# Performance work log

Measured on AMD Instinct MI355X. Metric: run time of the kernel, lower is better.

The kernel has to match this reference:

```python
import jax, jax.numpy as jnp
import numpy as np

HIDDEN = 2048
HEADS = 16
HEAD_DIM = HIDDEN // HEADS
BATCH = 2
SEQ = 2048
ROPE_BASE = 10000.0


def _rope_cos_sin(seq_len, head_dim, dtype):
    inv_freq = 1.0 / (ROPE_BASE ** (jnp.arange(0, head_dim, 2, dtype=jnp.float32) / head_dim))
    t = jnp.arange(seq_len, dtype=jnp.float32)
    freqs = jnp.outer(t, inv_freq)                 # [S, D/2]
    emb = jnp.concatenate([freqs, freqs], axis=-1)  # [S, D]
    return jnp.cos(emb).astype(dtype), jnp.sin(emb).astype(dtype)


def _rotate_half(x):
    x1, x2 = jnp.split(x, 2, axis=-1)
    return jnp.concatenate([-x2, x1], axis=-1)


def setup_inputs() -> dict:
    key = jax.random.key(0)
    ks = jax.random.split(key, 5)
    scale = 1.0 / np.sqrt(HIDDEN)
    return {
        "x": jax.random.normal(ks[0], (BATCH, SEQ, HIDDEN), dtype=jnp.float32),
        "Wq": jax.random.normal(ks[1], (HIDDEN, HIDDEN), dtype=jnp.float32) * scale,
        "Wk": jax.random.normal(ks[2], (HIDDEN, HIDDEN), dtype=jnp.float32) * scale,
        "Wv": jax.random.normal(ks[3], (HIDDEN, HIDDEN), dtype=jnp.float32) * scale,
        "Wo": jax.random.normal(ks[4], (HIDDEN, HIDDEN), dtype=jnp.float32) * scale,
    }


def reference(x, Wq, Wk, Wv, Wo):
    B, S, H = x.shape
    # projections (torch Linear: y = x @ W.T)
    q = jnp.einsum('bsh,oh->bso', x, Wq).reshape(B, S, HEADS, HEAD_DIM).transpose(0, 2, 1, 3)
    k = jnp.einsum('bsh,oh->bso', x, Wk).reshape(B, S, HEADS, HEAD_DIM).transpose(0, 2, 1, 3)
    v = jnp.einsum('bsh,oh->bso', x, Wv).reshape(B, S, HEADS, HEAD_DIM).transpose(0, 2, 1, 3)
    # RoPE
    cos, sin = _rope_cos_sin(S, HEAD_DIM, x.dtype)  # [S, D]
    cos = cos[None, None]  # [1,1,S,D]
    sin = sin[None, None]
    q = q * cos + _rotate_half(q) * sin
    k = k * cos + _rotate_half(k) * sin
    # attention scores [B, H, S, S]
    scale = HEAD_DIM ** -0.5
    scores = jnp.einsum('bhqd,bhkd->bhqk', q, k) * scale
    causal = jnp.triu(jnp.ones((S, S), dtype=bool), k=1)  # kv_len==seq -> diagonal=1
    scores = jnp.where(causal[None, None], -jnp.inf, scores)
    attn = jax.nn.softmax(scores.astype(jnp.float32), axis=-1).astype(q.dtype)
    # dropout is identity in eval mode
    out = jnp.einsum('bhqk,bhkd->bhqd', attn, v)  # [B,H,S,D]
    out = out.transpose(0, 2, 1, 3).reshape(B, S, H)
    return jnp.einsum('bsh,oh->bso', out, Wo)
```

## Files before the change

kernel.cpp:

```cpp
#include <hip/hip_runtime.h>
#include <hip/hip_bf16.h>
#include <cstdint>
#include <cstddef>

constexpr int HIDDEN = 2048;
constexpr int HEADS  = 16;
constexpr int HD     = 128;
constexpr int BATCH  = 2;
constexpr int SEQ    = 2048;
constexpr int MROWS  = BATCH * SEQ;

typedef __attribute__((ext_vector_type(8))) short bf16x8;
typedef __attribute__((ext_vector_type(4))) float f32x4;

__device__ __forceinline__ unsigned short f2bf(float f) {
  union { float f; unsigned int u; } c; c.f = f;
  unsigned int r = c.u + 0x7FFFu + ((c.u >> 16) & 1u);
  return (unsigned short)(r >> 16);
}
__device__ __forceinline__ unsigned short f2bft(float f) {
  union { float f; unsigned int u; } c; c.f = f;
  return (unsigned short)(c.u >> 16);
}
__device__ __forceinline__ float bf2f(unsigned short u) {
  union { unsigned int u; float f; } c; c.u = ((unsigned int)u) << 16;
  return c.f;
}

__device__ __forceinline__ void gload_lds16(const void* g, void* l) {
  __builtin_amdgcn_global_load_lds(
      (const __attribute__((address_space(1))) void*)g,
      (__attribute__((address_space(3))) void*)l, 16, 0, 0);
}

__global__ void k_cvt_all(const float* __restrict__ x,
                          const float* __restrict__ w0, const float* __restrict__ w1,
                          const float* __restrict__ w2, const float* __restrict__ w3,
                          unsigned short* __restrict__ out) {
  constexpr int N4X = MROWS * HIDDEN / 4;
  constexpr int N4W = HIDDEN * HIDDEN / 4;
  int idx = blockIdx.x * 256 + threadIdx.x;
  const float* src;
  int off;
  if (idx < N4X) { src = x; off = idx; }
  else {
    int j = idx - N4X;
    int seg = j >> 20;
    off = j & (N4W - 1);
    src = (seg == 0) ? w0 : (seg == 1) ? w1 : (seg == 2) ? w2 : w3;
  }
  float4 v = reinterpret_cast<const float4*>(src)[off];
  ushort4 o;
  o.x = f2bf(v.x); o.y = f2bf(v.y); o.z = f2bf(v.z); o.w = f2bf(v.w);
  reinterpret_cast<ushort4*>(out)[idx] = o;
}

constexpr int GK  = 2048;
constexpr int GNT = GK / 64;

template<int MODE, int BM, int BN>
__global__ __launch_bounds__(512)
__attribute__((amdgpu_waves_per_eu(2)))
void k_gemm256(const unsigned short* __restrict__ A,
               const unsigned short* __restrict__ Bm,
               void* __restrict__ Cout) {
  constexpr int ABYTES = BM * 64 * 2;
  constexpr int BBYTES = BN * 64 * 2;
  constexpr int AG = BM / 64;
  constexpr int BG = BN / 64;
  constexpr int G  = AG + BG;
  constexpr int MI = BM / 32;
  constexpr int NI = BN / 64;

  __shared__ char lds[2 * (ABYTES + BBYTES)];
  char* ldsA = lds;
  char* ldsB = lds + 2 * ABYTES;

  const int t    = threadIdx.x;
  const int lane = t & 63;
  const int w    = t >> 6;
  const int wr   = w >> 2;
  const int wc   = w & 3;
  const int l15  = lane & 15, lg = lane >> 4;

  const int orig = blockIdx.x;
  const int wg   = (orig & 7) * 32 + (orig >> 3);
  const int m0   = (wg >> 4) * BM;
  const int n0   = (wg & 15) * BN;

  const int rowA = t >> 3;
  const int xsel = ((t & 7) ^ (rowA & 7)) * 8;
  const unsigned short* aS = A  + (size_t)(m0 + rowA) * GK + xsel;
  const unsigned short* bS = Bm + (size_t)(n0 + rowA) * GK + xsel;
  char* aD = ldsA + t * 16;
  char* bD = ldsB + t * 16;

#define STAGEG(buf, kt) do {                                       \
    const unsigned short* ap = aS + (kt) * 64;                     \
    const unsigned short* bp = bS + (kt) * 64;                     \
    char* ad = aD + (buf) * ABYTES;                                \
    char* bd = bD + (buf) * BBYTES;                                \
    _Pragma("unroll")                                              \
    for (int g = 0; g < AG; ++g)                                   \
      gload_lds16(ap + (size_t)g * 64 * GK, ad + g * 8192);        \
    _Pragma("unroll")                                              \
    for (int g = 0; g < BG; ++g)                                   \
      gload_lds16(bp + (size_t)g * 64 * GK, bd + g * 8192);        \
  } while (0)

  const int xr  = (l15 & 7) << 4;
  const int vo0 = (lg * 16) ^ xr;
  const int vo1 = (64 + lg * 16) ^ xr;
  const char* aR = ldsA + wr * (BM / 2) * 128 + l15 * 128;
  const char* bR = ldsB + wc * (BN / 4) * 128 + l15 * 128;

  f32x4 acc[MI][NI];
#pragma unroll
  for (int mi = 0; mi < MI; ++mi)
#pragma unroll
    for (int ni = 0; ni < NI; ++ni)
#pragma unroll
      for (int r = 0; r < 4; ++r) acc[mi][ni][r] = 0.f;

  STAGEG(0, 0);
  STAGEG(1, 1);
  asm volatile("s_waitcnt vmcnt(%0)" :: "i"(G) : "memory");
  __builtin_amdgcn_s_barrier();
  asm volatile("" ::: "memory");

#pragma unroll 1
  for (int kt = 0; kt < GNT; ++kt) {
    const int buf = kt & 1;
    const char* a = aR + buf * ABYTES;
    const char* b = bR + buf * BBYTES;

    bf16x8 af0[MI], bf0[NI];
#pragma unroll
    for (int mi = 0; mi < MI; ++mi)
      af0[mi] = *reinterpret_cast<const bf16x8*>(a + mi * 2048 + vo0);
#pragma unroll
    for (int ni = 0; ni < NI; ++ni)
      bf0[ni] = *reinterpret_cast<const bf16x8*>(b + ni * 2048 + vo0);
    __builtin_amdgcn_s_setprio(1);
#pragma unroll
    for (int mi = 0; mi < MI; ++mi)
#pragma unroll
      for (int ni = 0; ni < NI; ++ni)
        acc[mi][ni] = __builtin_amdgcn_mfma_f32_16x16x32_bf16(af0[mi], bf0[ni], acc[mi][ni], 0, 0, 0);
    __builtin_amdgcn_s_setprio(0);

    bf16x8 af1[MI], bf1[NI];
#pragma unroll
    for (int mi = 0; mi < MI; ++mi)
      af1[mi] = *reinterpret_cast<const bf16x8*>(a + mi * 2048 + vo1);
#pragma unroll
    for (int ni = 0; ni < NI; ++ni)
      bf1[ni] = *reinterpret_cast<const bf16x8*>(b + ni * 2048 + vo1);

    asm volatile("s_waitcnt lgkmcnt(0)" ::: "memory");
    __builtin_amdgcn_s_barrier();
    asm volatile("" ::: "memory");

    if (kt < GNT - 2) STAGEG(buf, kt + 2);

    __builtin_amdgcn_s_setprio(1);
#pragma unroll
    for (int mi = 0; mi < MI; ++mi)
#pragma unroll
      for (int ni = 0; ni < NI; ++ni)
        acc[mi][ni] = __builtin_amdgcn_mfma_f32_16x16x32_bf16(af1[mi], bf1[ni], acc[mi][ni], 0, 0, 0);
    __builtin_amdgcn_s_setprio(0);

    if (kt < GNT - 2) asm volatile("s_waitcnt vmcnt(%0)" :: "i"(G) : "memory");
    else              asm volatile("s_waitcnt vmcnt(0)" ::: "memory");
    __builtin_amdgcn_s_barrier();
    asm volatile("" ::: "memory");
  }
#undef STAGEG

#pragma unroll
  for (int mi = 0; mi < MI; ++mi) {
#pragma unroll
    for (int ni = 0; ni < NI; ++ni) {
#pragma unroll
      for (int r = 0; r < 4; ++r) {
        int row = m0 + wr * (BM / 2) + mi * 16 + lg * 4 + r;
        int col = n0 + wc * (BN / 4) + ni * 16 + l15;
        float v = acc[mi][ni][r];
        if (MODE == 2) {
          reinterpret_cast<float*>(Cout)[(size_t)row * 2048 + col] = v;
        } else if (MODE == 0) {
          int bb = row >> 11, s = row & (SEQ - 1);
          int which = col >> 11;
          int hc = col & 2047;
          int h = hc >> 7, d = hc & (HD - 1);
          size_t addr = (size_t)which * ((size_t)MROWS * HIDDEN)
                      + ((size_t)(bb * HEADS + h) * SEQ + s) * HD + d;
          reinterpret_cast<unsigned short*>(Cout)[addr] = f2bf(v);
        } else {
          int h = row >> 7, d = row & (HD - 1);
          int bb = col >> 11, s = col & (SEQ - 1);
          size_t addr = ((size_t)(bb * HEADS + h) * HD + d) * SEQ + s;
          reinterpret_cast<unsigned short*>(Cout)[addr] = f2bf(v);
        }
      }
    }
  }
}

constexpr float QSCALE = 0.08838834764831845f * 1.4426950408889634f;

__global__ void k_rope(unsigned short* __restrict__ Qb, unsigned short* __restrict__ Kb) {
  int idx = blockIdx.x * 256 + threadIdx.x;
  int c  = idx & 7;
  int s  = (idx >> 3) & (SEQ - 1);
  int bh = idx >> 14;
  size_t base = ((size_t)bh * SEQ + s) * HD + c * 8;

  bf16x8 ql = *reinterpret_cast<const bf16x8*>(Qb + base);
  bf16x8 qh = *reinterpret_cast<const bf16x8*>(Qb + base + 64);
  bf16x8 kl = *reinterpret_cast<const bf16x8*>(Kb + base);
  bf16x8 kh = *reinterpret_cast<const bf16x8*>(Kb + base + 64);
  bf16x8 qlo, qho, klo, kho;
#pragma unroll
  for (int j = 0; j < 8; ++j) {
    float d   = (float)(c * 8 + j);
    float ang = (float)s * expf(d * -0.14391156511756683f);
    float sn, cs;
    __sincosf(ang, &sn, &cs);
    float a0 = bf2f((unsigned short)ql[j]), a1 = bf2f((unsigned short)qh[j]);
    qlo[j] = (short)f2bf((a0 * cs - a1 * sn) * QSCALE);
    qho[j] = (short)f2bf((a1 * cs + a0 * sn) * QSCALE);
    float b0 = bf2f((unsigned short)kl[j]), b1 = bf2f((unsigned short)kh[j]);
    klo[j] = (short)f2bf(b0 * cs - b1 * sn);
    kho[j] = (short)f2bf(b1 * cs + b0 * sn);
  }
  *reinterpret_cast<bf16x8*>(Qb + base)      = qlo;
  *reinterpret_cast<bf16x8*>(Qb + base + 64) = qho;
  *reinterpret_cast<bf16x8*>(Kb + base)      = klo;
  *reinterpret_cast<bf16x8*>(Kb + base + 64) = kho;
}

constexpr int QB  = 128;
constexpr int KVB = 64;
constexpr int NQT = SEQ / QB;

__global__ __launch_bounds__(512)
__attribute__((amdgpu_waves_per_eu(4, 4)))
void k_attn(const unsigned short* __restrict__ Q,
            const unsigned short* __restrict__ Kk,
            const unsigned short* __restrict__ Vt,
            unsigned short* __restrict__ O) {
  __shared__ char lds[2 * 16384 + 2 * 16384 + 16384];
  char* Ks = lds;
  char* Vs = lds + 2 * 16384;
  char* Ps = lds + 4 * 16384;

  const int t    = threadIdx.x;
  const int lane = t & 63;
  const int w    = t >> 6;
  const int l15  = lane & 15, lg = lane >> 4;
  const int bh   = blockIdx.y;
  const int b    = bh >> 4, h = bh & 15;
  const int qt   = (bh >= HEADS) ? (NQT - 1 - (int)blockIdx.x) : (int)blockIdx.x;
  const int q0b  = qt * QB;
  const int q0w  = q0b + w * 16;
  const int qw_hi = q0w + 15;

  const unsigned short* Qb = Q  + (size_t)bh * SEQ * HD;
  const unsigned short* Kb = Kk + (size_t)bh * SEQ * HD;
  const unsigned short* Vb = Vt + (size_t)bh * HD * SEQ;

  bf16x8 qf[4];
#pragma unroll
  for (int c = 0; c < 4; ++c)
    qf[c] = *reinterpret_cast<const bf16x8*>(Qb + (size_t)(q0w + l15) * HD + c * 32 + lg * 8);

  float mrow[4], lpart[4];
  f32x4 oacc[8];
#pragma unroll
  for (int r = 0; r < 4; ++r) { mrow[r] = -1e30f; lpart[r] = 0.f; }
#pragma unroll
  for (int dt = 0; dt < 8; ++dt)
#pragma unroll
    for (int r = 0; r < 4; ++r) oacc[dt][r] = 0.f;

  const int sp     = t * 16;
  const int srow   = sp >> 8;
  const int scolb  = (sp & 255) ^ ((srow & 7) << 4);
  const unsigned short* ksrc2 = Kb + (size_t)srow * HD + (scolb >> 1);
  char* kdst2 = Ks + sp;

  const int vrow  = t >> 3;
  const int vcolb = ((t & 7) << 4) ^ ((vrow & 7) << 4);
  const unsigned short* vsrc = Vb + (size_t)vrow * SEQ + (vcolb >> 1);
  char* vdst = Vs + t * 16;

  const int nb = q0b / KVB + 2;

  gload_lds16(ksrc2, kdst2);
  gload_lds16(ksrc2 + (size_t)32 * HD, kdst2 + 8192);
  gload_lds16(vsrc, vdst);
  gload_lds16(vsrc + (size_t)64 * SEQ, vdst + 8192);
  __syncthreads();

  int cur = 0;
  for (int kb = 0; kb < nb; ++kb) {
    const int kv0 = kb * KVB;
    if (kb + 1 < nb) {
      const int nxt = kv0 + KVB;
      char* nk = kdst2 + (cur ^ 1) * 16384;
      char* nv = vdst  + (cur ^ 1) * 16384;
      gload_lds16(ksrc2 + (size_t)nxt * HD, nk);
      gload_lds16(ksrc2 + (size_t)(nxt + 32) * HD, nk + 8192);
      gload_lds16(vsrc + nxt, nv);
      gload_lds16(vsrc + (size_t)64 * SEQ + nxt, nv + 8192);
    }

    if (kv0 <= qw_hi) {
      const char* Kc = Ks + cur * 16384;
      const char* Vc = Vs + cur * 16384;
      f32x4 sc[4];
#pragma unroll
      for (int tt = 0; tt < 4; ++tt)
#pragma unroll
        for (int r = 0; r < 4; ++r) sc[tt][r] = 0.f;
      __builtin_amdgcn_s_setprio(1);
#pragma unroll
      for (int tt = 0; tt < 4; ++tt) {
        const int kr = tt * 16 + l15;
        const int xr = (kr & 7) << 4;
#pragma unroll
        for (int c = 0; c < 4; ++c) {
          bf16x8 kf = *reinterpret_cast<const bf16x8*>(
              Kc + kr * 256 + ((c * 64 + lg * 16) ^ xr));
          sc[tt] = __builtin_amdgcn_mfma_f32_16x16x32_bf16(qf[c], kf, sc[tt], 0, 0, 0);
        }
      }
      __builtin_amdgcn_s_setprio(0);

      const bool full = (kv0 + KVB - 1 <= q0w);
#pragma unroll
      for (int r = 0; r < 4; ++r) {
        const int qg = q0w + lg * 4 + r;
        float v0 = sc[0][r], v1 = sc[1][r];
        float v2 = sc[2][r], v3 = sc[3][r];
        if (!full) {
          if (kv0 +      l15 > qg) v0 = -1e30f;
          if (kv0 + 16 + l15 > qg) v1 = -1e30f;
          if (kv0 + 32 + l15 > qg) v2 = -1e30f;
          if (kv0 + 48 + l15 > qg) v3 = -1e30f;
        }
        float pm = fmaxf(fmaxf(v0, v1), fmaxf(v2, v3));
        if (__any(pm > mrow[r] + 11.5f)) {
          float pmr = pm;
          pmr = fmaxf(pmr, __shfl_xor(pmr, 1));
          pmr = fmaxf(pmr, __shfl_xor(pmr, 2));
          pmr = fmaxf(pmr, __shfl_xor(pmr, 4));
          pmr = fmaxf(pmr, __shfl_xor(pmr, 8));
          float mn = fmaxf(mrow[r], pmr);
          float al = exp2f(mrow[r] - mn);
          lpart[r] *= al;
#pragma unroll
          for (int dt = 0; dt < 8; ++dt) oacc[dt][r] *= al;
          mrow[r] = mn;
        }
        float p0 = exp2f(v0 - mrow[r]);
        float p1 = exp2f(v1 - mrow[r]);
        float p2 = exp2f(v2 - mrow[r]);
        float p3 = exp2f(v3 - mrow[r]);
        lpart[r] += (p0 + p1) + (p2 + p3);
        const int prow = lg * 4 + r;
        const int xpr  = (prow & 7) << 4;
        char* pw = Ps + w * 2048 + prow * 128;
        *reinterpret_cast<unsigned short*>(pw + (((0 * 32) + l15 * 2) ^ xpr)) = f2bft(p0);
        *reinterpret_cast<unsigned short*>(pw + (((1 * 32) + l15 * 2) ^ xpr)) = f2bft(p1);
        *reinterpret_cast<unsigned short*>(pw + (((2 * 32) + l15 * 2) ^ xpr)) = f2bft(p2);
        *reinterpret_cast<unsigned short*>(pw + (((3 * 32) + l15 * 2) ^ xpr)) = f2bft(p3);
      }
      asm volatile("s_waitcnt lgkmcnt(0)" ::: "memory");

      const int xq = (l15 & 7) << 4;
      const char* pr = Ps + w * 2048 + l15 * 128;
      bf16x8 pa0 = *reinterpret_cast<const bf16x8*>(pr + ((0  + lg * 16) ^ xq));
      bf16x8 pa1 = *reinterpret_cast<const bf16x8*>(pr + ((64 + lg * 16) ^ xq));
      const int xv = (l15 & 7) << 4;
      __builtin_amdgcn_s_setprio(1);
#pragma unroll
      for (int dt = 0; dt < 8; ++dt) {
        const char* vrl = Vc + (dt * 16 + l15) * 128;
        bf16x8 vf0 = *reinterpret_cast<const bf16x8*>(vrl + ((lg * 16) ^ xv));
        bf16x8 vf1 = *reinterpret_cast<const bf16x8*>(vrl + ((64 + lg * 16) ^ xv));
        oacc[dt] = __builtin_amdgcn_mfma_f32_16x16x32_bf16(pa0, vf0, oacc[dt], 0, 0, 0);
        oacc[dt] = __builtin_amdgcn_mfma_f32_16x16x32_bf16(pa1, vf1, oacc[dt], 0, 0, 0);
      }
      __builtin_amdgcn_s_setprio(0);
    }
    __syncthreads();
    cur ^= 1;
  }

  float inv[4];
#pragma unroll
  for (int r = 0; r < 4; ++r) {
    float ls = lpart[r];
    ls += __shfl_xor(ls, 1);
    ls += __shfl_xor(ls, 2);
    ls += __shfl_xor(ls, 4);
    ls += __shfl_xor(ls, 8);
    inv[r] = 1.0f / ls;
  }
#pragma unroll
  for (int dt = 0; dt < 8; ++dt) {
#pragma unroll
    for (int r = 0; r < 4; ++r) {
      int qg = q0w + lg * 4 + r;
      int dv = dt * 16 + l15;
      O[((size_t)(b * SEQ + qg) * HEADS + h) * HD + dv] = f2bf(oacc[dt][r] * inv[r]);
    }
  }
}

extern "C" void kernel_launch(void* const* d_in, const int* in_sizes, int n_in,
                              void* d_out, int out_size, void* d_ws, size_t ws_size,
                              hipStream_t stream) {
  (void)in_sizes; (void)n_in; (void)out_size; (void)ws_size;
  const float* x  = (const float*)d_in[0];
  const float* Wq = (const float*)d_in[1];
  const float* Wk = (const float*)d_in[2];
  const float* Wv = (const float*)d_in[3];
  const float* Wo = (const float*)d_in[4];
  float* out = (float*)d_out;

  unsigned short* xb  = (unsigned short*)d_ws;
  unsigned short* wqb = xb  + (size_t)MROWS * HIDDEN;
  unsigned short* wkb = wqb + (size_t)HIDDEN * HIDDEN;
  unsigned short* wvb = wkb + (size_t)HIDDEN * HIDDEN;
  unsigned short* wob = wvb + (size_t)HIDDEN * HIDDEN;
  unsigned short* Qb  = wob + (size_t)HIDDEN * HIDDEN;
  unsigned short* Kb  = Qb  + (size_t)MROWS * HIDDEN;
  unsigned short* Vtb = Kb  + (size_t)MROWS * HIDDEN;
  unsigned short* Ob  = Vtb + (size_t)MROWS * HIDDEN;
  (void)wkb;

  constexpr int CVT_THREADS = (MROWS * HIDDEN + 4 * HIDDEN * HIDDEN) / 4;
  k_cvt_all<<<CVT_THREADS / 256, 256, 0, stream>>>(x, Wq, Wk, Wv, Wo, xb);

  k_gemm256<0, 256, 256><<<256, 512, 0, stream>>>(xb, wqb, Qb);
  k_gemm256<3, 128, 256><<<256, 512, 0, stream>>>(wvb, xb, Vtb);

  k_rope<<<(BATCH * HEADS * SEQ * 8) / 256, 256, 0, stream>>>(Qb, Kb);

  k_attn<<<dim3(SEQ / QB, BATCH * HEADS), 512, 0, stream>>>(Qb, Kb, Vtb, Ob);

  k_gemm256<2, 256, 128><<<256, 512, 0, stream>>>(Ob, wob, out);
}
```

Before: 240.8 us.

## Add specialized QK projection GEMM with staggered A/B prefetch and split-phase MFMA

Replaces the generic 256x256 templated GEMM for the fused Q/K projection with a hand-scheduled kernel. It staggers global-to-LDS loads of A and B across different points in the k-loop and splits each k-step into four half-phases, each a batch of LDS fragment reads followed by MFMAs under raised priority. The goal is to hide global load latency and interleave LDS reads with matrix work better than the old single-phase schedule. In exchange it adds more barriers per iteration and duplicates the GEMM code.

```diff
diff --git a/kernel.cpp b/kernel.cpp
--- a/kernel.cpp
+++ b/kernel.cpp
@@ -58,6 +58,176 @@
 constexpr int GK  = 2048;
 constexpr int GNT = GK / 64;
 
+__global__ __launch_bounds__(512)
+__attribute__((amdgpu_waves_per_eu(2)))
+void k_gemmQK(const unsigned short* __restrict__ A,
+              const unsigned short* __restrict__ Bm,
+              unsigned short* __restrict__ Cout) {
+  constexpr int ABYTES = 32768, BBYTES = 32768;
+  __shared__ char lds[131072];
+  char* ldsA = lds;
+  char* ldsB = lds + 2 * ABYTES;
+
+  const int t    = threadIdx.x;
+  const int lane = t & 63;
+  const int w    = t >> 6;
+  const int wr   = w >> 2;
+  const int wc   = w & 3;
+  const int l15  = lane & 15, lg = lane >> 4;
+
+  const int orig = blockIdx.x;
+  const int wg   = (orig & 7) * 32 + (orig >> 3);
+  const int m0   = (wg >> 4) * 256;
+  const int n0   = (wg & 15) * 256;
+
+  const int rowA = t >> 3;
+  const int xsel = ((t & 7) ^ (rowA & 7)) * 8;
+  const unsigned short* aS = A  + (size_t)(m0 + rowA) * GK + xsel;
+  const unsigned short* bS = Bm + (size_t)(n0 + rowA) * GK + xsel;
+  char* aD = ldsA + t * 16;
+  char* bD = ldsB + t * 16;
+
+#define STAGE_A(buf, kt) do {                                      \
+    const unsigned short* ap = aS + (kt) * 64;                     \
+    char* ad = aD + (buf) * ABYTES;                                \
+    gload_lds16(ap,                ad);                            \
+    gload_lds16(ap +  64 * GK,     ad + 8192);                    \
+    gload_lds16(ap + 128 * GK,     ad + 16384);                   \
+    gload_lds16(ap + 192 * GK,     ad + 24576);                   \
+  } while (0)
+#define STAGE_B(buf, kt) do {                                      \
+    const unsigned short* bp = bS + (kt) * 64;                     \
+    char* bd = bD + (buf) * BBYTES;                                \
+    gload_lds16(bp,                bd);                            \
+    gload_lds16(bp +  64 * GK,     bd + 8192);                    \
+    gload_lds16(bp + 128 * GK,     bd + 16384);                   \
+    gload_lds16(bp + 192 * GK,     bd + 24576);                   \
+  } while (0)
+
+  const int xr  = (l15 & 7) << 4;
+  const int vo0 = (lg * 16) ^ xr;
+  const int vo1 = (64 + lg * 16) ^ xr;
+  const char* aR = ldsA + wr * 16384 + l15 * 128;
+  const char* bR = ldsB + wc * 8192  + l15 * 128;
+
+  f32x4 acc[8][4];
+#pragma unroll
+  for (int mi = 0; mi < 8; ++mi)
+#pragma unroll
+    for (int ni = 0; ni < 4; ++ni)
+#pragma unroll
+      for (int r = 0; r < 4; ++r) acc[mi][ni][r] = 0.f;
+
+  STAGE_B(0, 0);
+  STAGE_A(0, 0);
+  STAGE_B(1, 1);
+  asm volatile("s_waitcnt vmcnt(4)" ::: "memory");
+  __builtin_amdgcn_s_barrier();
+  asm volatile("" ::: "memory");
+
+#pragma unroll 2
+  for (int kt = 0; kt < GNT; ++kt) {
+    const int buf = kt & 1;
+    const char* a = aR + buf * ABYTES;
+    const char* b = bR + buf * BBYTES;
+    bf16x8 bf[4], af[4], ag[4];
+
+#pragma unroll
+    for (int ni = 0; ni < 4; ++ni)
+      bf[ni] = *reinterpret_cast<const bf16x8*>(b + ni * 2048 + vo0);
+#pragma unroll
+    for (int mi = 0; mi < 4; ++mi)
+      af[mi] = *reinterpret_cast<const bf16x8*>(a + mi * 2048 + vo0);
+    if (kt + 1 < GNT) STAGE_A(buf ^ 1, kt + 1);
+    __builtin_amdgcn_s_barrier();
+    asm volatile("s_waitcnt lgkmcnt(0)" ::: "memory");
+    __builtin_amdgcn_s_setprio(1);
+#pragma unroll
+    for (int mi = 0; mi < 4; ++mi)
+#pragma unroll
+      for (int ni = 0; ni < 4; ++ni)
+        acc[mi][ni] = __builtin_amdgcn_mfma_f32_16x16x32_bf16(af[mi], bf[ni], acc[mi][ni], 0, 0, 0);
+    __builtin_amdgcn_s_setprio(0);
+    __builtin_amdgcn_s_barrier();
+    asm volatile("" ::: "memory");
+
+#pragma unroll
+    for (int mi = 0; mi < 4; ++mi)
+      ag[mi] = *reinterpret_cast<const bf16x8*>(a + (mi + 4) * 2048 + vo0);
+    __builtin_amdgcn_s_barrier();
+    asm volatile("s_waitcnt lgkmcnt(0)" ::: "memory");
+    __builtin_amdgcn_s_setprio(1);
+#pragma unroll
+    for (int mi = 0; mi < 4; ++mi)
+#pragma unroll
+      for (int ni = 0; ni < 4; ++ni)
+        acc[mi + 4][ni] = __builtin_amdgcn_mfma_f32_16x16x32_bf16(ag[mi], bf[ni], acc[mi + 4][ni], 0, 0, 0);
+    __builtin_amdgcn_s_setprio(0);
+    __builtin_amdgcn_s_barrier();
+    asm volatile("" ::: "memory");
+
+#pragma unroll
+    for (int ni = 0; ni < 4; ++ni)
+      bf[ni] = *reinterpret_cast<const bf16x8*>(b + ni * 2048 + vo1);
+#pragma unroll
+    for (int mi = 0; mi < 4; ++mi)
+      af[mi] = *reinterpret_cast<const bf16x8*>(a + mi * 2048 + vo1);
+    __builtin_amdgcn_s_barrier();
+    asm volatile("s_waitcnt lgkmcnt(0)" ::: "memory");
+    __builtin_amdgcn_s_setprio(1);
+#pragma unroll
+    for (int mi = 0; mi < 4; ++mi)
+#pragma unroll
+      for (int ni = 0; ni < 4; ++ni)
+        acc[mi][ni] = __builtin_amdgcn_mfma_f32_16x16x32_bf16(af[mi], bf[ni], acc[mi][ni], 0, 0, 0);
+    __builtin_amdgcn_s_setprio(0);
+    __builtin_amdgcn_s_barrier();
+    asm volatile("" ::: "memory");
+
+#pragma unroll
+    for (int mi = 0; mi < 4; ++mi)
+      ag[mi] = *reinterpret_cast<const bf16x8*>(a + (mi + 4) * 2048 + vo1);
+    if (kt + 2 < GNT) {
+      STAGE_B(buf, kt + 2);
+      asm volatile("s_waitcnt vmcnt(4)" ::: "memory");
+    } else {
+      asm volatile("s_waitcnt vmcnt(0)" ::: "memory");
+    }
+    __builtin_amdgcn_s_barrier();
+    asm volatile("s_waitcnt lgkmcnt(0)" ::: "memory");
+    __builtin_amdgcn_s_setprio(1);
+#pragma unroll
+    for (int mi = 0; mi < 4; ++mi)
+#pragma unroll
+      for (int ni = 0; ni < 4; ++ni)
+        acc[mi + 4][ni] = __builtin_amdgcn_mfma_f32_16x16x32_bf16(ag[mi], bf[ni], acc[mi + 4][ni], 0, 0, 0);
+    __builtin_amdgcn_s_setprio(0);
+    __builtin_amdgcn_s_barrier();
+    asm volatile("" ::: "memory");
+  }
+#undef STAGE_A
+#undef STAGE_B
+
+#pragma unroll
+  for (int mi = 0; mi < 8; ++mi) {
+#pragma unroll
+    for (int ni = 0; ni < 4; ++ni) {
+#pragma unroll
+      for (int r = 0; r < 4; ++r) {
+        int row = m0 + wr * 128 + mi * 16 + lg * 4 + r;
+        int col = n0 + wc * 64 + ni * 16 + l15;
+        int bb = row >> 11, s = row & (SEQ - 1);
+        int which = col >> 11;
+        int hc = col & 2047;
+        int h = hc >> 7, d = hc & (HD - 1);
+        size_t addr = (size_t)which * ((size_t)MROWS * HIDDEN)
+                    + ((size_t)(bb * HEADS + h) * SEQ + s) * HD + d;
+        Cout[addr] = f2bf(acc[mi][ni][r]);
+      }
+    }
+  }
+}
+
 template<int MODE, int BM, int BN>
 __global__ __launch_bounds__(512)
 __attribute__((amdgpu_waves_per_eu(2)))
@@ -189,14 +359,6 @@
         float v = acc[mi][ni][r];
         if (MODE == 2) {
           reinterpret_cast<float*>(Cout)[(size_t)row * 2048 + col] = v;
-        } else if (MODE == 0) {
-          int bb = row >> 11, s = row & (SEQ - 1);
-          int which = col >> 11;
-          int hc = col & 2047;
-          int h = hc >> 7, d = hc & (HD - 1);
-          size_t addr = (size_t)which * ((size_t)MROWS * HIDDEN)
-                      + ((size_t)(bb * HEADS + h) * SEQ + s) * HD + d;
-          reinterpret_cast<unsigned short*>(Cout)[addr] = f2bf(v);
         } else {
           int h = row >> 7, d = row & (HD - 1);
           int bb = col >> 11, s = col & (SEQ - 1);
@@ -446,7 +608,7 @@
   constexpr int CVT_THREADS = (MROWS * HIDDEN + 4 * HIDDEN * HIDDEN) / 4;
   k_cvt_all<<<CVT_THREADS / 256, 256, 0, stream>>>(x, Wq, Wk, Wv, Wo, xb);
 
-  k_gemm256<0, 256, 256><<<256, 512, 0, stream>>>(xb, wqb, Qb);
+  k_gemmQK<<<256, 512, 0, stream>>>(xb, wqb, Qb);
   k_gemm256<3, 128, 256><<<256, 512, 0, stream>>>(wvb, xb, Vtb);
 
   k_rope<<<(BATCH * HEADS * SEQ * 8) / 256, 256, 0, stream>>>(Qb, Kb);
```

Result: no change. 241.4 us (+0.3%).

## Transpose QK^T MFMA to keep P in registers via permlane swaps; remap blocks

Applied to the files above, without the earlier changes.

Swaps the MFMA operands so each lane holds scores for a single query row, which turns the softmax max/sum into per-lane reductions plus two cross-group shuffles. The P tile is packed to bf16 with v_cvt_pk_bf16_f32 and rearranged with v_permlane32/16_swap into the A-operand layout, so the LDS round trip and its wait are gone. The P buffer is dropped from shared memory. Blocks are also remapped so that consecutive blocks interleave heads and reverse the q-tile order, to spread causal work more evenly across CUs. The cost is extra permlane and shuffle instructions, a dependency on gfx950-specific instructions, and a P rounding that now uses the round-to-nearest pack instead of truncation.

```diff
diff --git a/kernel.cpp b/kernel.cpp
--- a/kernel.cpp
+++ b/kernel.cpp
@@ -12,15 +12,12 @@
 
 typedef __attribute__((ext_vector_type(8))) short bf16x8;
 typedef __attribute__((ext_vector_type(4))) float f32x4;
+typedef __attribute__((ext_vector_type(4))) unsigned u32x4;
 
 __device__ __forceinline__ unsigned short f2bf(float f) {
   union { float f; unsigned int u; } c; c.f = f;
   unsigned int r = c.u + 0x7FFFu + ((c.u >> 16) & 1u);
   return (unsigned short)(r >> 16);
-}
-__device__ __forceinline__ unsigned short f2bft(float f) {
-  union { float f; unsigned int u; } c; c.f = f;
-  return (unsigned short)(c.u >> 16);
 }
 __device__ __forceinline__ float bf2f(unsigned short u) {
   union { unsigned int u; float f; } c; c.u = ((unsigned int)u) << 16;
@@ -251,18 +248,22 @@
             const unsigned short* __restrict__ Kk,
             const unsigned short* __restrict__ Vt,
             unsigned short* __restrict__ O) {
-  __shared__ char lds[2 * 16384 + 2 * 16384 + 16384];
+  __shared__ char lds[2 * 16384 + 2 * 16384];
   char* Ks = lds;
   char* Vs = lds + 2 * 16384;
-  char* Ps = lds + 4 * 16384;
 
   const int t    = threadIdx.x;
   const int lane = t & 63;
   const int w    = t >> 6;
   const int l15  = lane & 15, lg = lane >> 4;
-  const int bh   = blockIdx.y;
-  const int b    = bh >> 4, h = bh & 15;
-  const int qt   = (bh >= HEADS) ? (NQT - 1 - (int)blockIdx.x) : (int)blockIdx.x;
+
+  const int lin     = blockIdx.x + 16 * blockIdx.y;
+  const int pos     = lin >> 3;
+  const int logical = (lin & 7) * 64 + pos;
+  const int bh      = logical >> 4;
+  const int qt0     = logical & 15;
+  const int qt      = (pos < 32) ? qt0 : (15 - qt0);
+  const int b  = bh >> 4, h = bh & 15;
   const int q0b  = qt * QB;
   const int q0w  = q0b + w * 16;
   const int qw_hi = q0w + 15;
@@ -276,10 +277,8 @@
   for (int c = 0; c < 4; ++c)
     qf[c] = *reinterpret_cast<const bf16x8*>(Qb + (size_t)(q0w + l15) * HD + c * 32 + lg * 8);
 
-  float mrow[4], lpart[4];
+  float m = -1e30f, lpart = 0.f;
   f32x4 oacc[8];
-#pragma unroll
-  for (int r = 0; r < 4; ++r) { mrow[r] = -1e30f; lpart[r] = 0.f; }
 #pragma unroll
   for (int dt = 0; dt < 8; ++dt)
 #pragma unroll
@@ -334,56 +333,78 @@
         for (int c = 0; c < 4; ++c) {
           bf16x8 kf = *reinterpret_cast<const bf16x8*>(
               Kc + kr * 256 + ((c * 64 + lg * 16) ^ xr));
-          sc[tt] = __builtin_amdgcn_mfma_f32_16x16x32_bf16(qf[c], kf, sc[tt], 0, 0, 0);
+          sc[tt] = __builtin_amdgcn_mfma_f32_16x16x32_bf16(kf, qf[c], sc[tt], 0, 0, 0);
         }
       }
       __builtin_amdgcn_s_setprio(0);
 
       const bool full = (kv0 + KVB - 1 <= q0w);
-#pragma unroll
-      for (int r = 0; r < 4; ++r) {
-        const int qg = q0w + lg * 4 + r;
-        float v0 = sc[0][r], v1 = sc[1][r];
-        float v2 = sc[2][r], v3 = sc[3][r];
-        if (!full) {
-          if (kv0 +      l15 > qg) v0 = -1e30f;
-          if (kv0 + 16 + l15 > qg) v1 = -1e30f;
-          if (kv0 + 32 + l15 > qg) v2 = -1e30f;
-          if (kv0 + 48 + l15 > qg) v3 = -1e30f;
+      const int qg = q0w + l15;
+      if (!full) {
+        const int kvb = kv0 + lg * 4;
+#pragma unroll
+        for (int tt = 0; tt < 4; ++tt)
+#pragma unroll
+          for (int r = 0; r < 4; ++r)
+            if (kvb + tt * 16 + r > qg) sc[tt][r] = -1e30f;
+      }
+      float pm01 = fmaxf(fmaxf(sc[0][0], sc[0][1]), fmaxf(sc[0][2], sc[0][3]));
+      float pm11 = fmaxf(fmaxf(sc[1][0], sc[1][1]), fmaxf(sc[1][2], sc[1][3]));
+      float pm21 = fmaxf(fmaxf(sc[2][0], sc[2][1]), fmaxf(sc[2][2], sc[2][3]));
+      float pm31 = fmaxf(fmaxf(sc[3][0], sc[3][1]), fmaxf(sc[3][2], sc[3][3]));
+      float pm = fmaxf(fmaxf(pm01, pm11), fmaxf(pm21, pm31));
+      if (__any(pm > m + 11.5f)) {
+        float pmr = pm;
+        pmr = fmaxf(pmr, __shfl_xor(pmr, 16));
+        pmr = fmaxf(pmr, __shfl_xor(pmr, 32));
+        float mn = fmaxf(m, pmr);
+        float al = exp2f(m - mn);
+        lpart *= al;
+#pragma unroll
+        for (int r = 0; r < 4; ++r) {
+          float alr = __shfl(al, lg * 4 + r, 16);
+#pragma unroll
+          for (int dt = 0; dt < 8; ++dt) oacc[dt][r] *= alr;
         }
-        float pm = fmaxf(fmaxf(v0, v1), fmaxf(v2, v3));
-        if (__any(pm > mrow[r] + 11.5f)) {
-          float pmr = pm;
-          pmr = fmaxf(pmr, __shfl_xor(pmr, 1));
-          pmr = fmaxf(pmr, __shfl_xor(pmr, 2));
-          pmr = fmaxf(pmr, __shfl_xor(pmr, 4));
-          pmr = fmaxf(pmr, __shfl_xor(pmr, 8));
-          float mn = fmaxf(mrow[r], pmr);
-          float al = exp2f(mrow[r] - mn);
-          lpart[r] *= al;
-#pragma unroll
-          for (int dt = 0; dt < 8; ++dt) oacc[dt][r] *= al;
-          mrow[r] = mn;
+        m = mn;
+      }
+      float p[4][4];
+      float ps = 0.f;
+#pragma unroll
+      for (int tt = 0; tt < 4; ++tt)
+#pragma unroll
+        for (int r = 0; r < 4; ++r) {
+          p[tt][r] = exp2f(sc[tt][r] - m);
+          ps += p[tt][r];
         }
-        float p0 = exp2f(v0 - mrow[r]);
-        float p1 = exp2f(v1 - mrow[r]);
-        float p2 = exp2f(v2 - mrow[r]);
-        float p3 = exp2f(v3 - mrow[r]);
-        lpart[r] += (p0 + p1) + (p2 + p3);
-        const int prow = lg * 4 + r;
-        const int xpr  = (prow & 7) << 4;
-        char* pw = Ps + w * 2048 + prow * 128;
-        *reinterpret_cast<unsigned short*>(pw + (((0 * 32) + l15 * 2) ^ xpr)) = f2bft(p0);
-        *reinterpret_cast<unsigned short*>(pw + (((1 * 32) + l15 * 2) ^ xpr)) = f2bft(p1);
-        *reinterpret_cast<unsigned short*>(pw + (((2 * 32) + l15 * 2) ^ xpr)) = f2bft(p2);
-        *reinterpret_cast<unsigned short*>(pw + (((3 * 32) + l15 * 2) ^ xpr)) = f2bft(p3);
-      }
-      asm volatile("s_waitcnt lgkmcnt(0)" ::: "memory");
-
-      const int xq = (l15 & 7) << 4;
-      const char* pr = Ps + w * 2048 + l15 * 128;
-      bf16x8 pa0 = *reinterpret_cast<const bf16x8*>(pr + ((0  + lg * 16) ^ xq));
-      bf16x8 pa1 = *reinterpret_cast<const bf16x8*>(pr + ((64 + lg * 16) ^ xq));
+      lpart += ps;
+
+      unsigned cc[4][2];
+#pragma unroll
+      for (int tt = 0; tt < 4; ++tt) {
+        asm("v_cvt_pk_bf16_f32 %0, %1, %2" : "=v"(cc[tt][0]) : "v"(p[tt][0]), "v"(p[tt][1]));
+        asm("v_cvt_pk_bf16_f32 %0, %1, %2" : "=v"(cc[tt][1]) : "v"(p[tt][2]), "v"(p[tt][3]));
+      }
+      u32x4 u0, u1;
+      {
+        unsigned a0 = cc[0][0], b0 = cc[1][0];
+        asm("v_permlane32_swap_b32 %0, %1" : "+v"(a0), "+v"(b0));
+        asm("v_permlane16_swap_b32 %0, %1" : "+v"(a0), "+v"(b0));
+        unsigned a1 = cc[0][1], b1 = cc[1][1];
+        asm("v_permlane32_swap_b32 %0, %1" : "+v"(a1), "+v"(b1));
+        asm("v_permlane16_swap_b32 %0, %1" : "+v"(a1), "+v"(b1));
+        u0[0] = a0; u0[1] = a1; u0[2] = b0; u0[3] = b1;
+        unsigned a2 = cc[2][0], b2 = cc[3][0];
+        asm("v_permlane32_swap_b32 %0, %1" : "+v"(a2), "+v"(b2));
+        asm("v_permlane16_swap_b32 %0, %1" : "+v"(a2), "+v"(b2));
+        unsigned a3 = cc[2][1], b3 = cc[3][1];
+        asm("v_permlane32_swap_b32 %0, %1" : "+v"(a3), "+v"(b3));
+        asm("v_permlane16_swap_b32 %0, %1" : "+v"(a3), "+v"(b3));
+        u1[0] = a2; u1[1] = a3; u1[2] = b2; u1[3] = b3;
+      }
+      bf16x8 pa0 = __builtin_bit_cast(bf16x8, u0);
+      bf16x8 pa1 = __builtin_bit_cast(bf16x8, u1);
+
       const int xv = (l15 & 7) << 4;
       __builtin_amdgcn_s_setprio(1);
 #pragma unroll
@@ -400,23 +421,20 @@
     cur ^= 1;
   }
 
-  float inv[4];
-#pragma unroll
-  for (int r = 0; r < 4; ++r) {
-    float ls = lpart[r];
-    ls += __shfl_xor(ls, 1);
-    ls += __shfl_xor(ls, 2);
-    ls += __shfl_xor(ls, 4);
-    ls += __shfl_xor(ls, 8);
-    inv[r] = 1.0f / ls;
-  }
+  float ls = lpart;
+  ls += __shfl_xor(ls, 16);
+  ls += __shfl_xor(ls, 32);
+  float inv = 1.0f / ls;
+  float invr[4];
+#pragma unroll
+  for (int r = 0; r < 4; ++r) invr[r] = __shfl(inv, lg * 4 + r, 16);
 #pragma unroll
   for (int dt = 0; dt < 8; ++dt) {
 #pragma unroll
     for (int r = 0; r < 4; ++r) {
       int qg = q0w + lg * 4 + r;
       int dv = dt * 16 + l15;
-      O[((size_t)(b * SEQ + qg) * HEADS + h) * HD + dv] = f2bf(oacc[dt][r] * inv[r]);
+      O[((size_t)(b * SEQ + qg) * HEADS + h) * HD + dv] = f2bf(oacc[dt][r] * invr[r]);
     }
   }
 }
```

Result: faster. 232.9 us (-3.3%).
